# Kernel optimization log

Hardware: AMD Instinct MI355X
Metric: run time of the kernel (lower is better)

Reference implementation:

```python
import jax, jax.numpy as jnp
import numpy as np

NUM_GROUPS = 32
EPS = 1e-6


def group_norm(x, gamma, beta):
    # x: [b, c, h, w]
    b, c, h, w = x.shape
    g = NUM_GROUPS
    xg = x.reshape(b, g, c // g, h, w)
    mean = xg.mean(axis=(2, 3, 4), keepdims=True)
    var = xg.var(axis=(2, 3, 4), keepdims=True)
    xn = ((xg - mean) * jax.lax.rsqrt(var + EPS)).reshape(b, c, h, w)
    return xn * gamma[None, :, None, None] + beta[None, :, None, None]


def conv1x1(x, w, b):
    # x: [b, c, h, w], w: [out_c, in_c], b: [out_c]
    return jnp.einsum('bchw,oc->bohw', x, w) + b[None, :, None, None]


def setup_inputs() -> dict:
    key = jax.random.key(0)
    ks = jax.random.split(key, 11)
    B, C, H, W = 4, 512, 64, 64
    s = 1.0 / np.sqrt(C)
    inp = {
        'x': jax.random.normal(ks[0], (B, C, H, W), dtype=jnp.float32),
        'gn_gamma': jnp.ones((C,), dtype=jnp.float32),
        'gn_beta': jnp.zeros((C,), dtype=jnp.float32),
        'wq': jax.random.normal(ks[1], (C, C), dtype=jnp.float32) * s,
        'bq': jax.random.normal(ks[2], (C,), dtype=jnp.float32) * 0.01,
        'wk': jax.random.normal(ks[3], (C, C), dtype=jnp.float32) * s,
        'bk': jax.random.normal(ks[4], (C,), dtype=jnp.float32) * 0.01,
        'wv': jax.random.normal(ks[5], (C, C), dtype=jnp.float32) * s,
        'bv': jax.random.normal(ks[6], (C,), dtype=jnp.float32) * 0.01,
        'wo': jax.random.normal(ks[7], (C, C), dtype=jnp.float32) * s,
        'bo': jax.random.normal(ks[8], (C,), dtype=jnp.float32) * 0.01,
    }
    return inp


def reference(x, gn_gamma, gn_beta, wq, bq, wk, bk, wv, bv, wo, bo):
    b, c, h, w = x.shape
    h_ = group_norm(x, gn_gamma, gn_beta)
    q = conv1x1(h_, wq, bq).reshape(b, c, h * w)  # [b, c, n]
    k = conv1x1(h_, wk, bk).reshape(b, c, h * w)
    v = conv1x1(h_, wv, bv).reshape(b, c, h * w)
    scale = jnp.asarray(c, x.dtype) ** -0.5
    # attn[b, i, j] = softmax_j(q_i . k_j * scale)
    attn = jax.nn.softmax(jnp.einsum('bci,bcj->bij', q, k) * scale, axis=-1)
    # A[b, c, i] = sum_j attn[b, i, j] * v[b, c, j]
    A = jnp.einsum('bij,bcj->bci', attn, v).reshape(b, c, h, w)
    A = conv1x1(A, wo, bo)
    # NOTE: the original module multiplies (not adds) the input by the attention output
    return x * A
```

## Files before the change

### kernel.cpp

```cpp
#include <hip/hip_runtime.h>
#include <hip/hip_bf16.h>
#include <stdint.h>

typedef __bf16 bf16x8 __attribute__((ext_vector_type(8)));
typedef __bf16 bf16x4 __attribute__((ext_vector_type(4)));
typedef float f32x4 __attribute__((ext_vector_type(4)));

__device__ __forceinline__ void gload_lds16(const __bf16* g, __bf16* l) {
  __builtin_amdgcn_global_load_lds(
      (const __attribute__((address_space(1))) void*)g,
      (__attribute__((address_space(3))) void*)l, 16, 0, 0);
}

__global__ __launch_bounds__(256) void cvt4_kernel(const float* __restrict__ s0,
                                                   const float* __restrict__ s1,
                                                   const float* __restrict__ s2,
                                                   const float* __restrict__ s3,
                                                   __bf16* __restrict__ dst) {
  int i = blockIdx.x * 256 + threadIdx.x;
  const float* srcs[4] = {s0, s1, s2, s3};
  int m = i >> 18;
  dst[i] = (__bf16)srcs[m][i & 262143];
}

__global__ __launch_bounds__(256) void biascat_kernel(const float* __restrict__ bq,
                                                      const float* __restrict__ bk,
                                                      float* __restrict__ bqk) {
  int i = blockIdx.x * 256 + threadIdx.x;
  bqk[i] = (i < 512) ? bq[i] : bk[i - 512];
}

__global__ __launch_bounds__(256) void gn1a_kernel(const float* __restrict__ x,
                                                   __bf16* __restrict__ xbf,
                                                   float2* __restrict__ part) {
  const int tid = threadIdx.x;
  const size_t base4 = ((size_t)blockIdx.x * 8192) >> 2;
  const float4* x4 = (const float4*)x;
  bf16x4* o4 = (bf16x4*)xbf;

  float s1 = 0.f, s2 = 0.f;
#pragma unroll
  for (int j = 0; j < 8; ++j) {
    float4 t = x4[base4 + tid + j * 256];
    s1 += t.x + t.y + t.z + t.w;
    s2 += t.x * t.x + t.y * t.y + t.z * t.z + t.w * t.w;
    bf16x4 o;
    o[0] = (__bf16)t.x; o[1] = (__bf16)t.y; o[2] = (__bf16)t.z; o[3] = (__bf16)t.w;
    o4[base4 + tid + j * 256] = o;
  }
#pragma unroll
  for (int off = 32; off; off >>= 1) {
    s1 += __shfl_xor(s1, off);
    s2 += __shfl_xor(s2, off);
  }
  __shared__ float r1[4], r2[4];
  if ((tid & 63) == 0) { r1[tid >> 6] = s1; r2[tid >> 6] = s2; }
  __syncthreads();
  if (tid == 0)
    part[blockIdx.x] = float2{r1[0] + r1[1] + r1[2] + r1[3],
                              r2[0] + r2[1] + r2[2] + r2[3]};
}

__global__ __launch_bounds__(512) void gn1b_kernel(const float2* __restrict__ part,
                                                   const float* __restrict__ gamma,
                                                   const float* __restrict__ beta,
                                                   float2* __restrict__ gmbt) {
  const int b = blockIdx.x;
  const int t = threadIdx.x;
  __shared__ float sm[32], si[32];
  if (t < 32) {
    float s1 = 0.f, s2 = 0.f;
#pragma unroll
    for (int j = 0; j < 8; ++j) {
      float2 p = part[(b * 32 + t) * 8 + j];
      s1 += p.x; s2 += p.y;
    }
    const float mean = s1 * (1.f / 65536.f);
    const float var = s2 * (1.f / 65536.f) - mean * mean;
    sm[t] = mean;
    si[t] = rsqrtf(var + 1e-6f);
  }
  __syncthreads();
  const int g = t >> 4;
  const float gm = gamma[t] * si[g];
  gmbt[b * 512 + t] = float2{gm, beta[t] - sm[g] * gm};
}

__global__ __launch_bounds__(256) void gn2_kernel(const __bf16* __restrict__ xbf,
                                                  const float2* __restrict__ gmbt,
                                                  __bf16* __restrict__ hnT) {
  const int b = blockIdx.z;
  const int c0 = blockIdx.y * 64;
  const int n0 = blockIdx.x * 64;
  const int t = threadIdx.x;
  __shared__ __bf16 tile[64][72];

  {
    const int row = t >> 2;
    const int col = (t & 3) * 16;
    const __bf16* src = xbf + ((size_t)(b * 512 + c0 + row)) * 4096 + n0 + col;
    bf16x8 u0 = *(const bf16x8*)src;
    bf16x8 u1 = *(const bf16x8*)(src + 8);
    *(bf16x8*)&tile[row][col] = u0;
    *(bf16x8*)&tile[row][col + 8] = u1;
  }
  __syncthreads();
  {
    const int nrow = t >> 2;
    const int cc = (t & 3) * 16;
    bf16x8 o0, o1;
#pragma unroll
    for (int j = 0; j < 16; ++j) {
      const int c = c0 + cc + j;
      float2 s = gmbt[b * 512 + c];
      float val = (float)tile[cc + j][nrow] * s.x + s.y;
      if (j < 8) o0[j] = (__bf16)val; else o1[j - 8] = (__bf16)val;
    }
    __bf16* dst = hnT + ((size_t)b * 4096 + n0 + nrow) * 512 + c0 + cc;
    *(bf16x8*)dst = o0;
    *(bf16x8*)(dst + 8) = o1;
  }
}

__global__ __launch_bounds__(256) void rowsum_inv_kernel(const __bf16* __restrict__ P,
                                                         float* __restrict__ inv) {
  const int r = blockIdx.x * 4 + (threadIdx.x >> 6);
  const int lane = threadIdx.x & 63;
  const bf16x8* rp = (const bf16x8*)(P + (size_t)r * 4096);
  float s = 0.f;
#pragma unroll
  for (int j = 0; j < 8; ++j) {
    bf16x8 v = rp[lane + j * 64];
#pragma unroll
    for (int e = 0; e < 8; ++e) s += (float)v[e];
  }
#pragma unroll
  for (int off = 32; off; off >>= 1) s += __shfl_xor(s, off);
  if (lane == 0) inv[r] = 1.0f / s;
}

template <int BN, int BIAS, int EEXP, int RSCALE, int KC>
__global__ __launch_bounds__(512) void gemm8p_kernel(
    const __bf16* __restrict__ A, int lda, long long sA,
    const __bf16* __restrict__ Bm, int ldb, long long sB,
    __bf16* __restrict__ Out, int ldo, long long sO,
    const float* __restrict__ bias, const float* __restrict__ rowinv,
    float scale) {
  constexpr int NF = BN / 64;
  constexpr int NH = NF / 2;
  constexpr int BSLOT = BN * 32;
  constexpr int WN = BN / 4;
  constexpr int BST = WN + 8;
  __shared__ __bf16 sm[4 * 8192 + 4 * BSLOT];
  __bf16* smB = sm + 4 * 8192;

  const int gx = gridDim.x, gxy = gx * gridDim.y;
  const int nwg = gxy * gridDim.z;
  int bid = blockIdx.x + gx * blockIdx.y + gxy * blockIdx.z;
  bid = (bid & 7) * (nwg >> 3) + (bid >> 3);
  const int bz = bid / gxy;
  const int rem = bid - bz * gxy;
  const int by = rem / gx, bx = rem - by * gx;
  const int tm0 = by * 256, tn0 = bx * BN;

  const int t = threadIdx.x;
  const int lane = t & 63, wid = t >> 6;
  const int wr = wid >> 2, wc = wid & 3;

  const __bf16* Az = A + (size_t)bz * sA;
  const __bf16* Bz = Bm + (size_t)bz * sB;

  const int scol = ((t & 3) * 8) ^ (((t >> 3) & 3) * 8);
  const __bf16* gA0 = Az + (size_t)(tm0 + (t >> 2)) * lda + scol;
  const __bf16* gA1 = gA0 + (size_t)128 * lda;
  const __bf16* gB0 = Bz + (size_t)(tn0 + (t >> 2)) * ldb + scol;
  const __bf16* gB1 = gB0 + (size_t)128 * ldb;
  __bf16* dA = sm + t * 8;
  __bf16* dB = smB + t * 8;

  auto stageA = [&](int ks) {
    const int sl = ks & 3;
    gload_lds16(gA0 + ks * 32, dA + sl * 8192);
    gload_lds16(gA1 + ks * 32, dA + sl * 8192 + 4096);
  };
  auto stageB = [&](int ks) {
    const int sl = ks & 3;
    gload_lds16(gB0 + ks * 32, dB + sl * BSLOT);
    if constexpr (BN == 256) gload_lds16(gB1 + ks * 32, dB + sl * BSLOT + 4096);
  };
  auto vmw = [&] {
    if constexpr (BN == 256) asm volatile("s_waitcnt vmcnt(8)" ::: "memory");
    else                     asm volatile("s_waitcnt vmcnt(6)" ::: "memory");
  };

  const int lr = lane & 15;
  const int kb = ((lane >> 4) * 16) ^ ((lr & 6) << 3);
  const __bf16* rdA = sm + (((wr * 128 + lr) * 64 + kb) >> 1);
  const __bf16* rdB = smB + (((wc * WN + lr) * 64 + kb) >> 1);

  f32x4 acc[8][NF];
#pragma unroll
  for (int m = 0; m < 8; ++m)
#pragma unroll
    for (int n = 0; n < NF; ++n) acc[m][n] = f32x4{0.f, 0.f, 0.f, 0.f};
  bf16x8 av[8];

  auto rdAfr = [&](int sl) {
#pragma unroll
    for (int m = 0; m < 8; ++m)
      av[m] = *(const bf16x8*)(rdA + sl * 8192 + m * 512);
  };
  auto mmaPh = [&](int sl, int nh) {
    bf16x8 bv[NH];
#pragma unroll
    for (int j = 0; j < NH; ++j)
      bv[j] = *(const bf16x8*)(rdB + sl * BSLOT + (nh * NH + j) * 512);
    __builtin_amdgcn_s_barrier();
    __builtin_amdgcn_s_setprio(1);
#pragma unroll
    for (int m = 0; m < 8; ++m)
#pragma unroll
      for (int j = 0; j < NH; ++j)
        acc[m][nh * NH + j] = __builtin_amdgcn_mfma_f32_16x16x32_bf16(
            av[m], bv[j], acc[m][nh * NH + j], 0, 0, 0);
    __builtin_amdgcn_s_setprio(0);
    __builtin_amdgcn_s_barrier();
  };

  constexpr int TOT = KC / 32;
  constexpr int NIT = TOT / 4;

  stageA(0); stageB(0); stageA(1); stageB(1); stageA(2); stageB(2);
  vmw();
  __builtin_amdgcn_s_barrier();

  for (int it = 0; it < NIT - 1; ++it) {
    const int s3 = 4 * it + 3;
    rdAfr(0); stageA(s3);          mmaPh(0, 0);
    stageB(s3); vmw();             mmaPh(0, 1);
    rdAfr(1); stageA(s3 + 1);      mmaPh(1, 0);
    stageB(s3 + 1); vmw();         mmaPh(1, 1);
    rdAfr(2); stageA(s3 + 2);      mmaPh(2, 0);
    stageB(s3 + 2); vmw();         mmaPh(2, 1);
    rdAfr(3); stageA(s3 + 3);      mmaPh(3, 0);
    stageB(s3 + 3); vmw();         mmaPh(3, 1);
  }
  {
    const int s3 = TOT - 1;
    rdAfr(0); stageA(s3);          mmaPh(0, 0);
    stageB(s3); vmw();             mmaPh(0, 1);
    rdAfr(1);                      mmaPh(1, 0);
    if constexpr (BN == 256) asm volatile("s_waitcnt vmcnt(4)" ::: "memory");
    else                     asm volatile("s_waitcnt vmcnt(3)" ::: "memory");
    mmaPh(1, 1);
    rdAfr(2);                      mmaPh(2, 0);
    if constexpr (BN == 256) asm volatile("s_waitcnt vmcnt(2)" ::: "memory");
    else                     asm volatile("s_waitcnt vmcnt(1)" ::: "memory");
    mmaPh(2, 1);
    rdAfr(3);                      mmaPh(3, 0);
    asm volatile("s_waitcnt vmcnt(0)" ::: "memory");
    mmaPh(3, 1);
  }

  __bf16* bnc = sm + wid * 16 * BST;
  const int q4 = (lane >> 4) * 4;
  const int row0 = tm0 + wr * 128;
  const int wn = tn0 + wc * WN;
  float bcol[NF];
#pragma unroll
  for (int n = 0; n < NF; ++n) bcol[n] = BIAS ? bias[wn + n * 16 + lr] : 0.f;
#pragma unroll
  for (int m = 0; m < 8; ++m) {
    float ri[4];
    if constexpr (RSCALE) {
#pragma unroll
      for (int r = 0; r < 4; ++r)
        ri[r] = rowinv[(size_t)bz * 4096 + row0 + m * 16 + q4 + r];
    }
#pragma unroll
    for (int n = 0; n < NF; ++n)
#pragma unroll
      for (int r = 0; r < 4; ++r) {
        float val = acc[m][n][r] * scale + bcol[n];
        if constexpr (EEXP) val = exp2f(val * 1.44269504f);
        if constexpr (RSCALE) val *= ri[r];
        bnc[(q4 + r) * BST + n * 16 + lr] = (__bf16)val;
      }
    if constexpr (WN == 64) {
      const int rr = lane >> 3, c8 = (lane & 7) * 8;
      bf16x8 v0 = *(const bf16x8*)&bnc[rr * BST + c8];
      bf16x8 v1 = *(const bf16x8*)&bnc[(rr + 8) * BST + c8];
      __bf16* op = Out + (size_t)bz * sO +
                   (size_t)(row0 + m * 16 + rr) * ldo + wn + c8;
      *(bf16x8*)op = v0;
      *(bf16x8*)(op + (size_t)8 * ldo) = v1;
    } else {
      const int rr = lane >> 2, c8 = (lane & 3) * 8;
      bf16x8 v0 = *(const bf16x8*)&bnc[rr * BST + c8];
      __bf16* op = Out + (size_t)bz * sO +
                   (size_t)(row0 + m * 16 + rr) * ldo + wn + c8;
      *(bf16x8*)op = v0;
    }
  }
}

template <int EPI, int BIAS>
__global__ __launch_bounds__(256) void gemm_lds_kernel(
    const __bf16* __restrict__ A, int lda, long long sA,
    const __bf16* __restrict__ Bm, int ldb, long long sB,
    void* __restrict__ Out, int ldo, long long sO,
    const float* __restrict__ bias, const __bf16* __restrict__ xmul,
    long long sX, float scale, int K) {
  __shared__ __bf16 sTa[2][128 * 32];
  __shared__ __bf16 sTb[2][128 * 32];

  const int gx = gridDim.x, gxy = gx * gridDim.y;
  const int nwg = gxy * gridDim.z;
  int bid = blockIdx.x + gx * blockIdx.y + gxy * blockIdx.z;
  if ((nwg & 7) == 0) bid = (bid & 7) * (nwg >> 3) + (bid >> 3);
  const int bz = bid / gxy;
  const int rem = bid - bz * gxy;
  const int by = rem / gx;
  const int bx = rem - by * gx;

  const int tid = threadIdx.x;
  const int lane = tid & 63;
  const int wid = tid >> 6;
  const int wr = wid >> 1, wc = wid & 1;
  const int tm0 = by * 128, tn0 = bx * 128;
  const int lr = lane & 15, lk = (lane >> 4) * 8;

  const int ch0 = wid * 2;
  const int srow = lane >> 2;
  const int scol = (lane & 3) * 8;
  const __bf16* gA0 = A + (size_t)bz * sA + (size_t)(tm0 + ch0 * 16 + srow) * lda + scol;
  const __bf16* gB0 = Bm + (size_t)bz * sB + (size_t)(tn0 + ch0 * 16 + srow) * ldb + scol;
  const size_t stepA = (size_t)16 * lda, stepB = (size_t)16 * ldb;

  f32x4 acc[4][4];
#pragma unroll
  for (int i = 0; i < 4; ++i)
#pragma unroll
    for (int j = 0; j < 4; ++j) acc[i][j] = f32x4{0.f, 0.f, 0.f, 0.f};

  const int T = K >> 5;
  gload_lds16(gA0, &sTa[0][ch0 * 512]);
  gload_lds16(gA0 + stepA, &sTa[0][ch0 * 512 + 512]);
  gload_lds16(gB0, &sTb[0][ch0 * 512]);
  gload_lds16(gB0 + stepB, &sTb[0][ch0 * 512 + 512]);

  for (int tt = 0; tt < T; ++tt) {
    __syncthreads();
    const int cur = tt & 1;
    if (tt + 1 < T) {
      const __bf16* a = gA0 + (size_t)(tt + 1) * 32;
      const __bf16* b = gB0 + (size_t)(tt + 1) * 32;
      gload_lds16(a, &sTa[cur ^ 1][ch0 * 512]);
      gload_lds16(a + stepA, &sTa[cur ^ 1][ch0 * 512 + 512]);
      gload_lds16(b, &sTb[cur ^ 1][ch0 * 512]);
      gload_lds16(b + stepB, &sTb[cur ^ 1][ch0 * 512 + 512]);
    }
    const __bf16* fa = &sTa[cur][(wr * 64 + lr) * 32 + lk];
    const __bf16* fb = &sTb[cur][(wc * 64 + lr) * 32 + lk];
    bf16x8 a[4], b[4];
#pragma unroll
    for (int i = 0; i < 4; ++i) a[i] = *(const bf16x8*)(fa + i * 512);
#pragma unroll
    for (int j = 0; j < 4; ++j) b[j] = *(const bf16x8*)(fb + j * 512);
#pragma unroll
    for (int i = 0; i < 4; ++i)
#pragma unroll
      for (int j = 0; j < 4; ++j)
        acc[i][j] = __builtin_amdgcn_mfma_f32_16x16x32_bf16(a[i], b[j], acc[i][j], 0, 0, 0);
  }

  const int wm = tm0 + wr * 64, wn = tn0 + wc * 64;
#pragma unroll
  for (int i = 0; i < 4; ++i) {
#pragma unroll
    for (int r = 0; r < 4; ++r) {
      const int row = wm + i * 16 + (lane >> 4) * 4 + r;
#pragma unroll
      for (int j = 0; j < 4; ++j) {
        const int col = wn + j * 16 + lr;
        float val = acc[i][j][r] * scale;
        if (BIAS == 1) val += bias[col];
        if (BIAS == 2) val += bias[row];
        const size_t off = (size_t)bz * sO + (size_t)row * ldo + col;
        if (EPI == 0) {
          ((__bf16*)Out)[off] = (__bf16)val;
        } else if (EPI == 1) {
          ((float*)Out)[off] = val;
        } else {
          ((float*)Out)[off] = (float)xmul[(size_t)bz * sX + (size_t)row * ldo + col] * val;
        }
      }
    }
  }
}

extern "C" void kernel_launch(void* const* d_in, const int* in_sizes, int n_in,
                              void* d_out, int out_size, void* d_ws, size_t ws_size,
                              hipStream_t stream) {
  const int C = 512, N = 4096;
  const float* x = (const float*)d_in[0];
  const float* gng = (const float*)d_in[1];
  const float* gnb = (const float*)d_in[2];
  const float* wq = (const float*)d_in[3];
  const float* bq = (const float*)d_in[4];
  const float* wk = (const float*)d_in[5];
  const float* bk = (const float*)d_in[6];
  const float* wv = (const float*)d_in[7];
  const float* bv = (const float*)d_in[8];
  const float* wo = (const float*)d_in[9];
  const float* bo = (const float*)d_in[10];

  char* ws = (char*)d_ws;
  const size_t MB = 1ull << 20;
  const long long NC = (long long)N * C;
  const long long NN = (long long)N * N;
  const long long NQK = (long long)N * 1024;
  const bool batched = ws_size >= 194 * MB + 32768;

  __bf16 *S, *qkT, *a2T, *v, *xbf, *wqB;
  char* misc;
  if (batched) {
    S   = (__bf16*)(ws);
    qkT = (__bf16*)(ws + 128 * MB);
    a2T = qkT;
    v   = (__bf16*)(ws + 160 * MB);
    xbf = (__bf16*)(ws + 176 * MB);
    wqB = (__bf16*)(ws + 192 * MB);
    misc = ws + 194 * MB;
  } else {
    S   = (__bf16*)(ws);
    qkT = (__bf16*)(ws + 32 * MB);
    a2T = (__bf16*)(ws + 64 * MB);
    v   = (__bf16*)(ws + 80 * MB);
    xbf = (__bf16*)(ws + 96 * MB);
    wqB = (__bf16*)(ws + 112 * MB);
    misc = ws + 114 * MB;
  }
  __bf16* hnT = (__bf16*)ws;
  __bf16* wvB = wqB + 2 * 262144;
  __bf16* woB = wvB + 262144;
  float* bqk   = (float*)misc;
  float2* gmbt = (float2*)(misc + 4096);
  float2* part = (float2*)(misc + 20480);
  float* rowInv = (float*)d_out;

  const float scl = 0.044194173824159216f;

  cvt4_kernel<<<4096, 256, 0, stream>>>(wq, wk, wv, wo, wqB);
  biascat_kernel<<<4, 256, 0, stream>>>(bq, bk, bqk);
  gn1a_kernel<<<1024, 256, 0, stream>>>(x, xbf, part);
  gn1b_kernel<<<4, 512, 0, stream>>>(part, gng, gnb, gmbt);
  gn2_kernel<<<dim3(64, 8, 4), 256, 0, stream>>>(xbf, gmbt, hnT);

  gemm8p_kernel<256, 1, 0, 0, 512><<<dim3(4, 16, 4), 512, 0, stream>>>(
      hnT, C, NC, wqB, C, 0, qkT, 1024, NQK, bqk, nullptr, 1.f);
  gemm_lds_kernel<0, 2><<<dim3(32, 4, 4), 256, 0, stream>>>(
      wvB, C, 0, hnT, C, NC, v, N, NC, bv, nullptr, 0, 1.f, C);

  if (batched) {
    gemm8p_kernel<256, 0, 1, 0, 512><<<dim3(16, 16, 4), 512, 0, stream>>>(
        qkT, 1024, NQK, qkT + 512, 1024, NQK, S, N, NN, nullptr, nullptr, scl);
    rowsum_inv_kernel<<<4096, 256, 0, stream>>>(S, rowInv);
    gemm8p_kernel<128, 0, 0, 1, 4096><<<dim3(4, 16, 4), 512, 0, stream>>>(
        S, N, NN, v, N, NC, a2T, C, NC, nullptr, rowInv, 1.f);
  } else {
    for (int b = 0; b < 4; ++b) {
      gemm8p_kernel<256, 0, 1, 0, 512><<<dim3(16, 16, 1), 512, 0, stream>>>(
          qkT + (size_t)b * NQK, 1024, 0, qkT + (size_t)b * NQK + 512, 1024, 0,
          S, N, 0, nullptr, nullptr, scl);
      rowsum_inv_kernel<<<1024, 256, 0, stream>>>(S, rowInv);
      gemm8p_kernel<128, 0, 0, 1, 4096><<<dim3(4, 16, 1), 512, 0, stream>>>(
          S, N, 0, v + (size_t)b * NC, N, 0, a2T + (size_t)b * NC, C, 0,
          nullptr, rowInv, 1.f);
    }
  }

  gemm_lds_kernel<2, 2><<<dim3(32, 4, 4), 256, 0, stream>>>(
      woB, C, 0, a2T, C, NC, (float*)d_out, N, NC, bo, xbf, NC, 1.f, C);
}
```

Measured before the change: 274.1 us.

## Replace 4-stage GEMM with 6-slot ring pipeline and fixed 256x128 tiles

The templated 4-deep pipelined GEMM becomes a single 256x128 tile kernel with a 6-slot LDS ring buffer, prefetching 5 K-steps ahead and rolling the slot indices in a non-unrolled loop. QK projection and QK^T score GEMMs now use narrower N tiles, which doubles their grid sizes. The goal is deeper latency hiding and more workgroups, at the cost of less B-operand reuse per tile and more LDS per block, which may lower occupancy.

```diff
diff --git a/kernel.cpp b/kernel.cpp
--- a/kernel.cpp
+++ b/kernel.cpp
@@ -139,20 +139,19 @@
   if (lane == 0) inv[r] = 1.0f / s;
 }
 
-template <int BN, int BIAS, int EEXP, int RSCALE, int KC>
-__global__ __launch_bounds__(512) void gemm8p_kernel(
+template <int BIAS, int EEXP, int RSCALE, int KC>
+__global__ __launch_bounds__(512) void gemm6r_kernel(
     const __bf16* __restrict__ A, int lda, long long sA,
     const __bf16* __restrict__ Bm, int ldb, long long sB,
     __bf16* __restrict__ Out, int ldo, long long sO,
     const float* __restrict__ bias, const float* __restrict__ rowinv,
     float scale) {
-  constexpr int NF = BN / 64;
-  constexpr int NH = NF / 2;
-  constexpr int BSLOT = BN * 32;
-  constexpr int WN = BN / 4;
+  constexpr int ASLOT = 8192;
+  constexpr int BSLOT = 4096;
+  constexpr int WN = 32;
   constexpr int BST = WN + 8;
-  __shared__ __bf16 sm[4 * 8192 + 4 * BSLOT];
-  __bf16* smB = sm + 4 * 8192;
+  __shared__ __bf16 sm[6 * ASLOT + 6 * BSLOT];
+  __bf16* smB = sm + 6 * ASLOT;
 
   const int gx = gridDim.x, gxy = gx * gridDim.y;
   const int nwg = gxy * gridDim.z;
@@ -161,7 +160,7 @@
   const int bz = bid / gxy;
   const int rem = bid - bz * gxy;
   const int by = rem / gx, bx = rem - by * gx;
-  const int tm0 = by * 256, tn0 = bx * BN;
+  const int tm0 = by * 256, tn0 = bx * 128;
 
   const int t = threadIdx.x;
   const int lane = t & 63, wid = t >> 6;
@@ -174,23 +173,15 @@
   const __bf16* gA0 = Az + (size_t)(tm0 + (t >> 2)) * lda + scol;
   const __bf16* gA1 = gA0 + (size_t)128 * lda;
   const __bf16* gB0 = Bz + (size_t)(tn0 + (t >> 2)) * ldb + scol;
-  const __bf16* gB1 = gB0 + (size_t)128 * ldb;
   __bf16* dA = sm + t * 8;
   __bf16* dB = smB + t * 8;
 
-  auto stageA = [&](int ks) {
-    const int sl = ks & 3;
-    gload_lds16(gA0 + ks * 32, dA + sl * 8192);
-    gload_lds16(gA1 + ks * 32, dA + sl * 8192 + 4096);
+  auto stageA = [&](int ks, int sl) {
+    gload_lds16(gA0 + (size_t)ks * 32, dA + sl * ASLOT);
+    gload_lds16(gA1 + (size_t)ks * 32, dA + sl * ASLOT + 4096);
   };
-  auto stageB = [&](int ks) {
-    const int sl = ks & 3;
-    gload_lds16(gB0 + ks * 32, dB + sl * BSLOT);
-    if constexpr (BN == 256) gload_lds16(gB1 + ks * 32, dB + sl * BSLOT + 4096);
-  };
-  auto vmw = [&] {
-    if constexpr (BN == 256) asm volatile("s_waitcnt vmcnt(8)" ::: "memory");
-    else                     asm volatile("s_waitcnt vmcnt(6)" ::: "memory");
+  auto stageB = [&](int ks, int sl) {
+    gload_lds16(gB0 + (size_t)ks * 32, dB + sl * BSLOT);
   };
 
   const int lr = lane & 15;
@@ -198,77 +189,73 @@
   const __bf16* rdA = sm + (((wr * 128 + lr) * 64 + kb) >> 1);
   const __bf16* rdB = smB + (((wc * WN + lr) * 64 + kb) >> 1);
 
-  f32x4 acc[8][NF];
-#pragma unroll
-  for (int m = 0; m < 8; ++m)
-#pragma unroll
-    for (int n = 0; n < NF; ++n) acc[m][n] = f32x4{0.f, 0.f, 0.f, 0.f};
+  f32x4 acc[8][2];
+#pragma unroll
+  for (int m = 0; m < 8; ++m) {
+    acc[m][0] = f32x4{0.f, 0.f, 0.f, 0.f};
+    acc[m][1] = f32x4{0.f, 0.f, 0.f, 0.f};
+  }
   bf16x8 av[8];
 
   auto rdAfr = [&](int sl) {
 #pragma unroll
     for (int m = 0; m < 8; ++m)
-      av[m] = *(const bf16x8*)(rdA + sl * 8192 + m * 512);
+      av[m] = *(const bf16x8*)(rdA + sl * ASLOT + m * 512);
   };
   auto mmaPh = [&](int sl, int nh) {
-    bf16x8 bv[NH];
-#pragma unroll
-    for (int j = 0; j < NH; ++j)
-      bv[j] = *(const bf16x8*)(rdB + sl * BSLOT + (nh * NH + j) * 512);
+    bf16x8 bv = *(const bf16x8*)(rdB + sl * BSLOT + nh * 512);
     __builtin_amdgcn_s_barrier();
     __builtin_amdgcn_s_setprio(1);
 #pragma unroll
     for (int m = 0; m < 8; ++m)
-#pragma unroll
-      for (int j = 0; j < NH; ++j)
-        acc[m][nh * NH + j] = __builtin_amdgcn_mfma_f32_16x16x32_bf16(
-            av[m], bv[j], acc[m][nh * NH + j], 0, 0, 0);
+      acc[m][nh] = __builtin_amdgcn_mfma_f32_16x16x32_bf16(av[m], bv, acc[m][nh], 0, 0, 0);
     __builtin_amdgcn_s_setprio(0);
     __builtin_amdgcn_s_barrier();
   };
 
   constexpr int TOT = KC / 32;
-  constexpr int NIT = TOT / 4;
-
-  stageA(0); stageB(0); stageA(1); stageB(1); stageA(2); stageB(2);
-  vmw();
+
+  stageA(0, 0); stageB(0, 0);
+  stageA(1, 1); stageB(1, 1);
+  stageA(2, 2); stageB(2, 2);
+  stageA(3, 3); stageB(3, 3);
+  stageA(4, 4); stageB(4, 4);
+  asm volatile("s_waitcnt vmcnt(12)" ::: "memory");
   __builtin_amdgcn_s_barrier();
 
-  for (int it = 0; it < NIT - 1; ++it) {
-    const int s3 = 4 * it + 3;
-    rdAfr(0); stageA(s3);          mmaPh(0, 0);
-    stageB(s3); vmw();             mmaPh(0, 1);
-    rdAfr(1); stageA(s3 + 1);      mmaPh(1, 0);
-    stageB(s3 + 1); vmw();         mmaPh(1, 1);
-    rdAfr(2); stageA(s3 + 2);      mmaPh(2, 0);
-    stageB(s3 + 2); vmw();         mmaPh(2, 1);
-    rdAfr(3); stageA(s3 + 3);      mmaPh(3, 0);
-    stageB(s3 + 3); vmw();         mmaPh(3, 1);
-  }
-  {
-    const int s3 = TOT - 1;
-    rdAfr(0); stageA(s3);          mmaPh(0, 0);
-    stageB(s3); vmw();             mmaPh(0, 1);
-    rdAfr(1);                      mmaPh(1, 0);
-    if constexpr (BN == 256) asm volatile("s_waitcnt vmcnt(4)" ::: "memory");
-    else                     asm volatile("s_waitcnt vmcnt(3)" ::: "memory");
-    mmaPh(1, 1);
-    rdAfr(2);                      mmaPh(2, 0);
-    if constexpr (BN == 256) asm volatile("s_waitcnt vmcnt(2)" ::: "memory");
-    else                     asm volatile("s_waitcnt vmcnt(1)" ::: "memory");
-    mmaPh(2, 1);
-    rdAfr(3);                      mmaPh(3, 0);
-    asm volatile("s_waitcnt vmcnt(0)" ::: "memory");
-    mmaPh(3, 1);
-  }
+  int cs = 0;
+  int ss = 5;
+#pragma unroll 1
+  for (int s = 0; s < TOT - 5; ++s) {
+    rdAfr(cs); stageA(s + 5, ss);   mmaPh(cs, 0);
+    stageB(s + 5, ss);
+    asm volatile("s_waitcnt vmcnt(12)" ::: "memory");
+    mmaPh(cs, 1);
+    cs = (cs == 5) ? 0 : cs + 1;
+    ss = (ss == 5) ? 0 : ss + 1;
+  }
+  rdAfr(cs); mmaPh(cs, 0);
+  asm volatile("s_waitcnt vmcnt(9)" ::: "memory");
+  mmaPh(cs, 1); cs = (cs == 5) ? 0 : cs + 1;
+  rdAfr(cs); mmaPh(cs, 0);
+  asm volatile("s_waitcnt vmcnt(6)" ::: "memory");
+  mmaPh(cs, 1); cs = (cs == 5) ? 0 : cs + 1;
+  rdAfr(cs); mmaPh(cs, 0);
+  asm volatile("s_waitcnt vmcnt(3)" ::: "memory");
+  mmaPh(cs, 1); cs = (cs == 5) ? 0 : cs + 1;
+  rdAfr(cs); mmaPh(cs, 0);
+  asm volatile("s_waitcnt vmcnt(0)" ::: "memory");
+  mmaPh(cs, 1); cs = (cs == 5) ? 0 : cs + 1;
+  rdAfr(cs); mmaPh(cs, 0);
+  mmaPh(cs, 1);
 
   __bf16* bnc = sm + wid * 16 * BST;
   const int q4 = (lane >> 4) * 4;
   const int row0 = tm0 + wr * 128;
   const int wn = tn0 + wc * WN;
-  float bcol[NF];
-#pragma unroll
-  for (int n = 0; n < NF; ++n) bcol[n] = BIAS ? bias[wn + n * 16 + lr] : 0.f;
+  float bcol[2];
+  bcol[0] = BIAS ? bias[wn + lr] : 0.f;
+  bcol[1] = BIAS ? bias[wn + 16 + lr] : 0.f;
 #pragma unroll
   for (int m = 0; m < 8; ++m) {
     float ri[4];
@@ -278,7 +265,7 @@
         ri[r] = rowinv[(size_t)bz * 4096 + row0 + m * 16 + q4 + r];
     }
 #pragma unroll
-    for (int n = 0; n < NF; ++n)
+    for (int n = 0; n < 2; ++n)
 #pragma unroll
       for (int r = 0; r < 4; ++r) {
         float val = acc[m][n][r] * scale + bcol[n];
@@ -286,21 +273,11 @@
         if constexpr (RSCALE) val *= ri[r];
         bnc[(q4 + r) * BST + n * 16 + lr] = (__bf16)val;
       }
-    if constexpr (WN == 64) {
-      const int rr = lane >> 3, c8 = (lane & 7) * 8;
-      bf16x8 v0 = *(const bf16x8*)&bnc[rr * BST + c8];
-      bf16x8 v1 = *(const bf16x8*)&bnc[(rr + 8) * BST + c8];
-      __bf16* op = Out + (size_t)bz * sO +
-                   (size_t)(row0 + m * 16 + rr) * ldo + wn + c8;
-      *(bf16x8*)op = v0;
-      *(bf16x8*)(op + (size_t)8 * ldo) = v1;
-    } else {
-      const int rr = lane >> 2, c8 = (lane & 3) * 8;
-      bf16x8 v0 = *(const bf16x8*)&bnc[rr * BST + c8];
-      __bf16* op = Out + (size_t)bz * sO +
-                   (size_t)(row0 + m * 16 + rr) * ldo + wn + c8;
-      *(bf16x8*)op = v0;
-    }
+    const int rr = lane >> 2, c8 = (lane & 3) * 8;
+    bf16x8 v0 = *(const bf16x8*)&bnc[rr * BST + c8];
+    __bf16* op = Out + (size_t)bz * sO +
+                 (size_t)(row0 + m * 16 + rr) * ldo + wn + c8;
+    *(bf16x8*)op = v0;
   }
 }
 
@@ -457,24 +434,24 @@
   gn1b_kernel<<<4, 512, 0, stream>>>(part, gng, gnb, gmbt);
   gn2_kernel<<<dim3(64, 8, 4), 256, 0, stream>>>(xbf, gmbt, hnT);
 
-  gemm8p_kernel<256, 1, 0, 0, 512><<<dim3(4, 16, 4), 512, 0, stream>>>(
+  gemm6r_kernel<1, 0, 0, 512><<<dim3(8, 16, 4), 512, 0, stream>>>(
       hnT, C, NC, wqB, C, 0, qkT, 1024, NQK, bqk, nullptr, 1.f);
   gemm_lds_kernel<0, 2><<<dim3(32, 4, 4), 256, 0, stream>>>(
       wvB, C, 0, hnT, C, NC, v, N, NC, bv, nullptr, 0, 1.f, C);
 
   if (batched) {
-    gemm8p_kernel<256, 0, 1, 0, 512><<<dim3(16, 16, 4), 512, 0, stream>>>(
+    gemm6r_kernel<0, 1, 0, 512><<<dim3(32, 16, 4), 512, 0, stream>>>(
         qkT, 1024, NQK, qkT + 512, 1024, NQK, S, N, NN, nullptr, nullptr, scl);
     rowsum_inv_kernel<<<4096, 256, 0, stream>>>(S, rowInv);
-    gemm8p_kernel<128, 0, 0, 1, 4096><<<dim3(4, 16, 4), 512, 0, stream>>>(
+    gemm6r_kernel<0, 0, 1, 4096><<<dim3(4, 16, 4), 512, 0, stream>>>(
         S, N, NN, v, N, NC, a2T, C, NC, nullptr, rowInv, 1.f);
   } else {
     for (int b = 0; b < 4; ++b) {
-      gemm8p_kernel<256, 0, 1, 0, 512><<<dim3(16, 16, 1), 512, 0, stream>>>(
+      gemm6r_kernel<0, 1, 0, 512><<<dim3(32, 16, 1), 512, 0, stream>>>(
           qkT + (size_t)b * NQK, 1024, 0, qkT + (size_t)b * NQK + 512, 1024, 0,
           S, N, 0, nullptr, nullptr, scl);
       rowsum_inv_kernel<<<1024, 256, 0, stream>>>(S, rowInv);
-      gemm8p_kernel<128, 0, 0, 1, 4096><<<dim3(4, 16, 1), 512, 0, stream>>>(
+      gemm6r_kernel<0, 0, 1, 4096><<<dim3(4, 16, 1), 512, 0, stream>>>(
           S, N, 0, v + (size_t)b * NC, N, 0, a2T + (size_t)b * NC, C, 0,
           nullptr, rowInv, 1.f);
     }
```

New measurement: 303.2 us. 1.11x slower.

## Fuse softmax row-sum into PV GEMM via ones-MFMA and add 128x128 GEMM kernel

Applied to the files above, without the earlier changes.

Removes the separate rowsum_inv kernel. The P·V GEMM now computes each row sum of the exp scores with an extra MFMA against a vector of ones and normalizes in its epilogue, which avoids a full extra read of the 4096x4096 score matrix. A new 4-wave 128x128-tile GEMM kernel replaces the 8-wave kernel for the QK projection and the PV product. The score GEMM epilogue now writes bf16 values straight to global memory instead of staging them through LDS, so its stores are narrow and scattered.

```diff
diff --git a/kernel.cpp b/kernel.cpp
--- a/kernel.cpp
+++ b/kernel.cpp
@@ -122,35 +122,16 @@
   }
 }
 
-__global__ __launch_bounds__(256) void rowsum_inv_kernel(const __bf16* __restrict__ P,
-                                                         float* __restrict__ inv) {
-  const int r = blockIdx.x * 4 + (threadIdx.x >> 6);
-  const int lane = threadIdx.x & 63;
-  const bf16x8* rp = (const bf16x8*)(P + (size_t)r * 4096);
-  float s = 0.f;
-#pragma unroll
-  for (int j = 0; j < 8; ++j) {
-    bf16x8 v = rp[lane + j * 64];
-#pragma unroll
-    for (int e = 0; e < 8; ++e) s += (float)v[e];
-  }
-#pragma unroll
-  for (int off = 32; off; off >>= 1) s += __shfl_xor(s, off);
-  if (lane == 0) inv[r] = 1.0f / s;
-}
-
-template <int BN, int BIAS, int EEXP, int RSCALE, int KC>
+template <int BN, int BIAS, int EEXP, int KC>
 __global__ __launch_bounds__(512) void gemm8p_kernel(
     const __bf16* __restrict__ A, int lda, long long sA,
     const __bf16* __restrict__ Bm, int ldb, long long sB,
     __bf16* __restrict__ Out, int ldo, long long sO,
-    const float* __restrict__ bias, const float* __restrict__ rowinv,
-    float scale) {
+    const float* __restrict__ bias, float scale) {
   constexpr int NF = BN / 64;
   constexpr int NH = NF / 2;
   constexpr int BSLOT = BN * 32;
   constexpr int WN = BN / 4;
-  constexpr int BST = WN + 8;
   __shared__ __bf16 sm[4 * 8192 + 4 * BSLOT];
   __bf16* smB = sm + 4 * 8192;
 
@@ -257,50 +238,169 @@
     if constexpr (BN == 256) asm volatile("s_waitcnt vmcnt(2)" ::: "memory");
     else                     asm volatile("s_waitcnt vmcnt(1)" ::: "memory");
     mmaPh(2, 1);
-    rdAfr(3);                      mmaPh(3, 0);
+    rdAfr(3);
     asm volatile("s_waitcnt vmcnt(0)" ::: "memory");
+    mmaPh(3, 0);
     mmaPh(3, 1);
   }
+
+  const int q4 = (lane >> 4) * 4;
+  const int wnb = tn0 + wc * WN;
+  float bcol[NF];
+#pragma unroll
+  for (int n = 0; n < NF; ++n) bcol[n] = BIAS ? bias[wnb + n * 16 + lr] : 0.f;
+#pragma unroll
+  for (int m = 0; m < 8; ++m) {
+#pragma unroll
+    for (int r = 0; r < 4; ++r) {
+      const int row = tm0 + wr * 128 + m * 16 + q4 + r;
+      __bf16* orow = Out + (size_t)bz * sO + (size_t)row * ldo + wnb + lr;
+#pragma unroll
+      for (int n = 0; n < NF; ++n) {
+        float val = acc[m][n][r] * scale + bcol[n];
+        if constexpr (EEXP) val = exp2f(val * 1.44269504f);
+        orow[n * 16] = (__bf16)val;
+      }
+    }
+  }
+}
+
+template <int BIAS, int RSUM, int KC>
+__global__ __launch_bounds__(256) void gemm4w_kernel(
+    const __bf16* __restrict__ A, int lda, long long sA,
+    const __bf16* __restrict__ Bm, int ldb, long long sB,
+    __bf16* __restrict__ Out, int ldo, long long sO,
+    const float* __restrict__ bias, float scale) {
+  constexpr int SLOT = 4096;
+  constexpr int BST = 72;
+  __shared__ __bf16 sm[8 * SLOT];
+  __bf16* smB = sm + 4 * SLOT;
+
+  const int gx = gridDim.x, gxy = gx * gridDim.y;
+  const int nwg = gxy * gridDim.z;
+  int bid = blockIdx.x + gx * blockIdx.y + gxy * blockIdx.z;
+  bid = (bid & 7) * (nwg >> 3) + (bid >> 3);
+  const int bz = bid / gxy;
+  const int rem = bid - bz * gxy;
+  const int by = rem / gx, bx = rem - by * gx;
+  const int tm0 = by * 128, tn0 = bx * 128;
+
+  const int t = threadIdx.x;
+  const int lane = t & 63, wid = t >> 6;
+  const int wr = wid >> 1, wc = wid & 1;
+
+  const __bf16* Az = A + (size_t)bz * sA;
+  const __bf16* Bz = Bm + (size_t)bz * sB;
+
+  const int scol = ((t & 3) * 8) ^ (((t >> 3) & 3) * 8);
+  const __bf16* gA0 = Az + (size_t)(tm0 + (t >> 2)) * lda + scol;
+  const __bf16* gA1 = gA0 + (size_t)64 * lda;
+  const __bf16* gB0 = Bz + (size_t)(tn0 + (t >> 2)) * ldb + scol;
+  const __bf16* gB1 = gB0 + (size_t)64 * ldb;
+  __bf16* dA = sm + t * 8;
+  __bf16* dB = smB + t * 8;
+
+  auto stage = [&](int ks) {
+    const int sl = ks & 3;
+    gload_lds16(gA0 + (size_t)ks * 32, dA + sl * SLOT);
+    gload_lds16(gA1 + (size_t)ks * 32, dA + sl * SLOT + 2048);
+    gload_lds16(gB0 + (size_t)ks * 32, dB + sl * SLOT);
+    gload_lds16(gB1 + (size_t)ks * 32, dB + sl * SLOT + 2048);
+  };
+
+  const int lr = lane & 15;
+  const int kb = ((lane >> 4) * 16) ^ ((lr & 6) << 3);
+  const __bf16* rdA = sm + (((wr * 64 + lr) * 64 + kb) >> 1);
+  const __bf16* rdB = smB + (((wc * 64 + lr) * 64 + kb) >> 1);
+
+  f32x4 acc[4][4];
+#pragma unroll
+  for (int i = 0; i < 4; ++i)
+#pragma unroll
+    for (int j = 0; j < 4; ++j) acc[i][j] = f32x4{0.f, 0.f, 0.f, 0.f};
+  f32x4 acc1[4];
+#pragma unroll
+  for (int i = 0; i < 4; ++i) acc1[i] = f32x4{0.f, 0.f, 0.f, 0.f};
+  bf16x8 onesf;
+#pragma unroll
+  for (int e = 0; e < 8; ++e) onesf[e] = (__bf16)1.0f;
+
+  bf16x8 av[4], bv[4];
+
+  auto rdfr = [&](int sl) {
+#pragma unroll
+    for (int m = 0; m < 4; ++m) av[m] = *(const bf16x8*)(rdA + sl * SLOT + m * 512);
+#pragma unroll
+    for (int n = 0; n < 4; ++n) bv[n] = *(const bf16x8*)(rdB + sl * SLOT + n * 512);
+  };
+  auto mma16 = [&] {
+    __builtin_amdgcn_s_barrier();
+    __builtin_amdgcn_s_setprio(1);
+#pragma unroll
+    for (int m = 0; m < 4; ++m)
+#pragma unroll
+      for (int n = 0; n < 4; ++n)
+        acc[m][n] = __builtin_amdgcn_mfma_f32_16x16x32_bf16(av[m], bv[n], acc[m][n], 0, 0, 0);
+    if constexpr (RSUM) {
+#pragma unroll
+      for (int m = 0; m < 4; ++m)
+        acc1[m] = __builtin_amdgcn_mfma_f32_16x16x32_bf16(av[m], onesf, acc1[m], 0, 0, 0);
+    }
+    __builtin_amdgcn_s_setprio(0);
+  };
+
+  constexpr int TOT = KC / 32;
+
+  stage(0); stage(1); stage(2);
+  asm volatile("s_waitcnt vmcnt(8)" ::: "memory");
+  __builtin_amdgcn_s_barrier();
+
+#pragma unroll 1
+  for (int s = 0; s < TOT - 3; ++s) {
+    rdfr(s & 3);
+    stage(s + 3);
+    mma16();
+    asm volatile("s_waitcnt vmcnt(8)" ::: "memory");
+    __builtin_amdgcn_s_barrier();
+  }
+  rdfr((TOT - 3) & 3); mma16();
+  asm volatile("s_waitcnt vmcnt(4)" ::: "memory");
+  __builtin_amdgcn_s_barrier();
+  rdfr((TOT - 2) & 3); mma16();
+  asm volatile("s_waitcnt vmcnt(0)" ::: "memory");
+  __builtin_amdgcn_s_barrier();
+  rdfr((TOT - 1) & 3); mma16();
+  __builtin_amdgcn_s_barrier();
 
   __bf16* bnc = sm + wid * 16 * BST;
   const int q4 = (lane >> 4) * 4;
-  const int row0 = tm0 + wr * 128;
-  const int wn = tn0 + wc * WN;
-  float bcol[NF];
-#pragma unroll
-  for (int n = 0; n < NF; ++n) bcol[n] = BIAS ? bias[wn + n * 16 + lr] : 0.f;
-#pragma unroll
-  for (int m = 0; m < 8; ++m) {
+  const int row0 = tm0 + wr * 64;
+  const int wn = tn0 + wc * 64;
+  float bcol[4];
+#pragma unroll
+  for (int n = 0; n < 4; ++n) bcol[n] = BIAS ? bias[wn + n * 16 + lr] : 0.f;
+#pragma unroll
+  for (int m = 0; m < 4; ++m) {
     float ri[4];
-    if constexpr (RSCALE) {
-#pragma unroll
-      for (int r = 0; r < 4; ++r)
-        ri[r] = rowinv[(size_t)bz * 4096 + row0 + m * 16 + q4 + r];
-    }
-#pragma unroll
-    for (int n = 0; n < NF; ++n)
+    if constexpr (RSUM) {
+#pragma unroll
+      for (int r = 0; r < 4; ++r) ri[r] = 1.0f / acc1[m][r];
+    }
+#pragma unroll
+    for (int n = 0; n < 4; ++n)
 #pragma unroll
       for (int r = 0; r < 4; ++r) {
         float val = acc[m][n][r] * scale + bcol[n];
-        if constexpr (EEXP) val = exp2f(val * 1.44269504f);
-        if constexpr (RSCALE) val *= ri[r];
+        if constexpr (RSUM) val *= ri[r];
         bnc[(q4 + r) * BST + n * 16 + lr] = (__bf16)val;
       }
-    if constexpr (WN == 64) {
-      const int rr = lane >> 3, c8 = (lane & 7) * 8;
-      bf16x8 v0 = *(const bf16x8*)&bnc[rr * BST + c8];
-      bf16x8 v1 = *(const bf16x8*)&bnc[(rr + 8) * BST + c8];
-      __bf16* op = Out + (size_t)bz * sO +
-                   (size_t)(row0 + m * 16 + rr) * ldo + wn + c8;
-      *(bf16x8*)op = v0;
-      *(bf16x8*)(op + (size_t)8 * ldo) = v1;
-    } else {
-      const int rr = lane >> 2, c8 = (lane & 3) * 8;
-      bf16x8 v0 = *(const bf16x8*)&bnc[rr * BST + c8];
-      __bf16* op = Out + (size_t)bz * sO +
-                   (size_t)(row0 + m * 16 + rr) * ldo + wn + c8;
-      *(bf16x8*)op = v0;
-    }
+    const int rr = lane >> 3, c8 = (lane & 7) * 8;
+    bf16x8 v0 = *(const bf16x8*)&bnc[rr * BST + c8];
+    bf16x8 v1 = *(const bf16x8*)&bnc[(rr + 8) * BST + c8];
+    __bf16* op = Out + (size_t)bz * sO +
+                 (size_t)(row0 + m * 16 + rr) * ldo + wn + c8;
+    *(bf16x8*)op = v0;
+    *(bf16x8*)(op + (size_t)8 * ldo) = v1;
   }
 }
 
@@ -447,7 +547,6 @@
   float* bqk   = (float*)misc;
   float2* gmbt = (float2*)(misc + 4096);
   float2* part = (float2*)(misc + 20480);
-  float* rowInv = (float*)d_out;
 
   const float scl = 0.044194173824159216f;
 
@@ -457,26 +556,24 @@
   gn1b_kernel<<<4, 512, 0, stream>>>(part, gng, gnb, gmbt);
   gn2_kernel<<<dim3(64, 8, 4), 256, 0, stream>>>(xbf, gmbt, hnT);
 
-  gemm8p_kernel<256, 1, 0, 0, 512><<<dim3(4, 16, 4), 512, 0, stream>>>(
-      hnT, C, NC, wqB, C, 0, qkT, 1024, NQK, bqk, nullptr, 1.f);
+  gemm4w_kernel<1, 0, 512><<<dim3(8, 32, 4), 256, 0, stream>>>(
+      hnT, C, NC, wqB, C, 0, qkT, 1024, NQK, bqk, 1.f);
   gemm_lds_kernel<0, 2><<<dim3(32, 4, 4), 256, 0, stream>>>(
       wvB, C, 0, hnT, C, NC, v, N, NC, bv, nullptr, 0, 1.f, C);
 
   if (batched) {
-    gemm8p_kernel<256, 0, 1, 0, 512><<<dim3(16, 16, 4), 512, 0, stream>>>(
-        qkT, 1024, NQK, qkT + 512, 1024, NQK, S, N, NN, nullptr, nullptr, scl);
-    rowsum_inv_kernel<<<4096, 256, 0, stream>>>(S, rowInv);
-    gemm8p_kernel<128, 0, 0, 1, 4096><<<dim3(4, 16, 4), 512, 0, stream>>>(
-        S, N, NN, v, N, NC, a2T, C, NC, nullptr, rowInv, 1.f);
+    gemm8p_kernel<256, 0, 1, 512><<<dim3(16, 16, 4), 512, 0, stream>>>(
+        qkT, 1024, NQK, qkT + 512, 1024, NQK, S, N, NN, nullptr, scl);
+    gemm4w_kernel<0, 1, 4096><<<dim3(4, 32, 4), 256, 0, stream>>>(
+        S, N, NN, v, N, NC, a2T, C, NC, nullptr, 1.f);
   } else {
     for (int b = 0; b < 4; ++b) {
-      gemm8p_kernel<256, 0, 1, 0, 512><<<dim3(16, 16, 1), 512, 0, stream>>>(
+      gemm8p_kernel<256, 0, 1, 512><<<dim3(16, 16, 1), 512, 0, stream>>>(
           qkT + (size_t)b * NQK, 1024, 0, qkT + (size_t)b * NQK + 512, 1024, 0,
-          S, N, 0, nullptr, nullptr, scl);
-      rowsum_inv_kernel<<<1024, 256, 0, stream>>>(S, rowInv);
-      gemm8p_kernel<128, 0, 0, 1, 4096><<<dim3(4, 16, 1), 512, 0, stream>>>(
+          S, N, 0, nullptr, scl);
+      gemm4w_kernel<0, 1, 4096><<<dim3(4, 32, 1), 256, 0, stream>>>(
           S, N, 0, v + (size_t)b * NC, N, 0, a2T + (size_t)b * NC, C, 0,
-          nullptr, rowInv, 1.f);
+          nullptr, 1.f);
     }
   }
 
```

Measured after the change: 271.6 us. About the same (-0.9%).
